# Performance work log

Measured on AMD Instinct MI355X. Metric: run time of the kernel, lower is better.

Reference implementation:

```python
import jax, jax.numpy as jnp
import numpy as np

B, C, D, J = 8, 2048, 128, 128

def setup_inputs() -> dict:
    key = jax.random.key(0)
    ks = jax.random.split(key, 24)
    s = 0.02
    inp = {
        "operation_features": jax.random.normal(ks[0], (B, C, D), jnp.float32),
        "relations": jax.random.randint(ks[1], (B, C - 2, 2), 0, C, jnp.int64),
        "begins_idx": jax.random.randint(ks[2], (B, J), 0, C, jnp.int64),
        "ends_idx": jax.random.randint(ks[3], (B, J), 0, C, jnp.int64),
        "same_type_mask": (jax.random.uniform(ks[4], (B, C, C)) > 0.5).astype(jnp.float32),
        # BeginEndEncoder
        "W_begin": jax.random.normal(ks[5], (D, D), jnp.float32) * s,
        "b_begin": jnp.zeros((D,), jnp.float32),
        "W_end": jax.random.normal(ks[6], (D, D), jnp.float32) * s,
        "b_end": jnp.zeros((D,), jnp.float32),
        # OperationTimeRelationEncoder.mix: Linear(3D -> D)
        "W_mix3": jax.random.normal(ks[7], (3 * D, D), jnp.float32) * s,
        "b_mix3": jnp.zeros((D,), jnp.float32),
        # SelfAttention (hidden_dim = D)
        "W_qkv": jax.random.normal(ks[8], (D, 3 * D), jnp.float32) * s,
        "b_qkv": jnp.zeros((3 * D,), jnp.float32),
        "w_score": jax.random.normal(ks[9], (2 * D,), jnp.float32) * s,
        "b_score": jnp.zeros((), jnp.float32),
        "W_out": jax.random.normal(ks[10], (D, D), jnp.float32) * s,
        "b_out": jnp.zeros((D,), jnp.float32),
        # block mix: Linear(2D -> D)
        "W_mix2": jax.random.normal(ks[11], (2 * D, D), jnp.float32) * s,
        "b_mix2": jnp.zeros((D,), jnp.float32),
    }
    return inp

def _gather_ops(ops, idx):
    # ops: [B,C,D], idx: [B,M] -> [B,M,D]  (torch.gather along dim 1 with expanded index)
    Bb, _, Dd = ops.shape
    M = idx.shape[1]
    return jnp.take_along_axis(ops, jnp.broadcast_to(idx[:, :, None], (Bb, M, Dd)), axis=1)

def reference(operation_features, relations, begins_idx, ends_idx, same_type_mask,
              W_begin, b_begin, W_end, b_end, W_mix3, b_mix3,
              W_qkv, b_qkv, w_score, b_score, W_out, b_out, W_mix2, b_mix2):
    ops = operation_features
    Dd = ops.shape[-1]
    # --- OperationTimeRelationEncoder ---
    pred = _gather_ops(ops, relations[..., 0])      # [B,C-2,D]
    succ = _gather_ops(ops, relations[..., 1])      # [B,C-2,D]
    concated = jnp.concatenate([ops[:, :-2, :], pred, succ], axis=-1)  # [B,C-2,3D]
    mixed = concated @ W_mix3 + b_mix3              # [B,C-2,D]
    begin_f = _gather_ops(ops, begins_idx) @ W_begin + b_begin  # [B,J,D]
    end_f = _gather_ops(ops, ends_idx) @ W_end + b_end
    begin = jnp.mean(begin_f, axis=1)               # [B,D]
    end = jnp.mean(end_f, axis=1)
    seq = jnp.concatenate([mixed, begin[:, None, :], end[:, None, :]], axis=1)  # [B,C,D]
    # --- SelfAttention (GAT-style additive score, decomposed to avoid CxCx2h blowup) ---
    qkv = ops @ W_qkv + b_qkv                       # [B,C,3D]
    q, k, v = jnp.split(qkv, 3, axis=-1)
    sq = q @ w_score[:Dd]                           # [B,C]  q_i . w_q
    sk = k @ w_score[Dd:]                           # [B,C]  k_j . w_k
    scores = jax.nn.leaky_relu(sq[:, :, None] + sk[:, None, :] + b_score)  # [B,C,C]
    attn = jax.nn.softmax(scores * same_type_mask, axis=-1)                # multiplicative mask, as in torch
    weighted = jnp.einsum('bij,bjd->bid', attn, v)  # [B,C,D]
    same_type = weighted @ W_out + b_out            # [B,C,D]
    # --- final mix ---
    return jnp.concatenate([seq, same_type], axis=-1) @ W_mix2 + b_mix2  # [B,C,D]
```

## Files before the change

kernel.cpp:

```cpp
#include <hip/hip_runtime.h>
#include <cstddef>

typedef __bf16 bf16;
typedef __bf16 bf16x4 __attribute__((ext_vector_type(4)));
typedef __bf16 bf16x8 __attribute__((ext_vector_type(8)));
typedef float  f32x4  __attribute__((ext_vector_type(4)));

#define MFMA16(a, b, c) __builtin_amdgcn_mfma_f32_16x16x32_bf16((a), (b), (c), 0, 0, 0)

#define BB 8
#define CC 2048
#define DD 128
#define JJN 128

#define WS_PK    ((size_t)0)
#define WS_OATT  ((size_t)4194304)
#define WS_OPS16 ((size_t)8388608)
#define WS_SQF   ((size_t)12582912)
#define WS_SKF   ((size_t)12648448)
#define WS_G1T   ((size_t)12713984)
#define WS_G2T   ((size_t)12746752)
#define WS_G3T   ((size_t)12779520)
#define WS_WCT   ((size_t)12812288)
#define WS_GBT   ((size_t)12845056)
#define WS_GET   ((size_t)12877824)
#define WS_UQK   ((size_t)12910592)
#define WS_BBM   ((size_t)12911104)
#define WS_BBB   ((size_t)12911616)
#define WS_BBE   ((size_t)12912128)
#define WS_SC    ((size_t)12912640)

__global__ __launch_bounds__(256) void k_prepcast(
    const float* __restrict__ ops, bf16* __restrict__ ops16,
    const float* __restrict__ Wmix3, const float* __restrict__ Wmix2,
    const float* __restrict__ Wout,  const float* __restrict__ Wbegin,
    const float* __restrict__ Wend,  const float* __restrict__ Wqkv,
    const float* __restrict__ bqkv,  const float* __restrict__ wscore,
    const float* __restrict__ bscore,const float* __restrict__ bmix3,
    const float* __restrict__ bout,  const float* __restrict__ bmix2,
    const float* __restrict__ bbegin,const float* __restrict__ bend,
    bf16* __restrict__ G1T, bf16* __restrict__ G2T, bf16* __restrict__ G3T,
    bf16* __restrict__ WCT, bf16* __restrict__ GBT, bf16* __restrict__ GET,
    bf16* __restrict__ uqk, float* __restrict__ BBM, float* __restrict__ BBB,
    float* __restrict__ BBE, float* __restrict__ sc)
{
    __shared__ bf16  LshT[128 * 132];
    __shared__ float Rsh[128 * 8];
    int wg = blockIdx.x;
    int t  = threadIdx.x;

    if (wg < 1024) {
        size_t i = (size_t)wg * 256 + t;
        f32x4 a = *(const f32x4*)(ops + i * 8);
        f32x4 b = *(const f32x4*)(ops + i * 8 + 4);
        bf16x8 o;
        #pragma unroll
        for (int e = 0; e < 4; ++e) { o[e] = (bf16)a[e]; o[4 + e] = (bf16)b[e]; }
        *(bf16x8*)(ops16 + i * 8) = o;
        return;
    }
    if (wg < 1120) {
        int id  = wg - 1024;
        int mat = id >> 4, sub = id & 15;
        const float* L; const float* R; bf16* O;
        switch (mat) {
            case 0: L = Wmix3;           R = Wmix2;           O = G1T; break;
            case 1: L = Wmix3 + 128*128; R = Wmix2;           O = G2T; break;
            case 2: L = Wmix3 + 256*128; R = Wmix2;           O = G3T; break;
            case 3: L = Wout;            R = Wmix2 + 128*128; O = WCT; break;
            case 4: L = Wbegin;          R = Wmix2;           O = GBT; break;
            default:L = Wend;            R = Wmix2;           O = GET; break;
        }
        int e0 = sub * 8;
        #pragma unroll
        for (int pass = 0; pass < 16; ++pass) {
            int idx = pass * 256 + t;
            int d   = idx >> 5;
            int f0  = (idx & 31) * 4;
            f32x4 v = *(const f32x4*)(L + d * 128 + f0);
            #pragma unroll
            for (int jj = 0; jj < 4; ++jj)
                LshT[(f0 + jj) * 132 + d] = (bf16)v[jj];
        }
        #pragma unroll
        for (int pass = 0; pass < 4; ++pass) {
            int idx = pass * 256 + t;
            int f   = idx >> 3;
            int ee  = idx & 7;
            Rsh[f * 8 + ee] = R[f * 128 + e0 + ee];
        }
        __syncthreads();
        int ee = t >> 5;
        int e  = e0 + ee;
        int d0 = (t & 31) * 4;
        float s[4] = {0.f, 0.f, 0.f, 0.f};
        for (int f = 0; f < 128; ++f) {
            bf16x4 lv = *(const bf16x4*)&LshT[f * 132 + d0];
            float rv = Rsh[f * 8 + ee];
            #pragma unroll
            for (int dd = 0; dd < 4; ++dd)
                s[dd] += (float)lv[dd] * rv;
        }
        #pragma unroll
        for (int dd = 0; dd < 4; ++dd)
            O[e * 128 + d0 + dd] = (bf16)s[dd];
        return;
    }
    if (t < 128) {
        int d = t;
        float su = 0.f, sk_ = 0.f;
        for (int e2 = 0; e2 < 128; ++e2) {
            su  += Wqkv[d*384 + e2]       * wscore[e2];
            sk_ += Wqkv[d*384 + 128 + e2] * wscore[128 + e2];
        }
        uqk[d]       = (bf16)su;
        uqk[128 + d] = (bf16)sk_;
        int e = d;
        float bm = 0.f, bon = 0.f, bb_ = 0.f, be_ = 0.f;
        for (int f = 0; f < 128; ++f) {
            float w2a = Wmix2[f*128 + e];
            float w2b = Wmix2[(128+f)*128 + e];
            bm  += bmix3[f]  * w2a;
            bon += bout[f]   * w2b;
            bb_ += bbegin[f] * w2a;
            be_ += bend[f]   * w2a;
        }
        float bm2 = bmix2[e];
        BBM[e] = bm  + bon + bm2;
        BBB[e] = bb_ + bon + bm2;
        BBE[e] = be_ + bon + bm2;
    } else if (t == 128) {
        float cq = 0.f, ck = 0.f;
        for (int e2 = 0; e2 < 128; ++e2) {
            cq += bqkv[e2]       * wscore[e2];
            ck += bqkv[128 + e2] * wscore[128 + e2];
        }
        sc[0] = cq + bscore[0];
        sc[1] = ck;
    }
}

__global__ __launch_bounds__(256) void k_v(
    const bf16* __restrict__ ops16, const float* __restrict__ Wqkv,
    const float* __restrict__ bqkv, const bf16* __restrict__ uqk,
    const float* __restrict__ sc,
    bf16* __restrict__ PK, float* __restrict__ sqf, float* __restrict__ skf)
{
    __shared__ bf16 A[144 * 136];
    int b  = blockIdx.x >> 4;
    int jt = (blockIdx.x & 15) * 128;
    int t  = threadIdx.x;
    #pragma unroll
    for (int pass = 0; pass < 16; ++pass) {
        int idx = pass * 256 + t;
        int d   = idx >> 5;
        int n0  = (idx & 31) * 4;
        f32x4 v = *(const f32x4*)(Wqkv + d*384 + 256 + n0);
        #pragma unroll
        for (int jj = 0; jj < 4; ++jj)
            A[(n0 + jj)*136 + d] = (bf16)v[jj];
    }
    {
        int row = t >> 7, col = t & 127;
        A[(128 + row)*136 + col] = uqk[row*128 + col];
    }
    for (int idx = t; idx < 14*136; idx += 256)
        A[130*136 + idx] = (bf16)0.f;
    __syncthreads();

    int lane = t & 63, w = t >> 6;
    int m = lane & 15, q = lane >> 4;
    f32x4 acc[9][2];
    #pragma unroll
    for (int rb = 0; rb < 9; ++rb)
        #pragma unroll
        for (int cb = 0; cb < 2; ++cb)
            acc[rb][cb] = {0.f, 0.f, 0.f, 0.f};

    const bf16* opsb = ops16 + (size_t)b * CC * DD;
    #pragma unroll
    for (int kc = 0; kc < 4; ++kc) {
        bf16x8 bfr[2];
        #pragma unroll
        for (int cb = 0; cb < 2; ++cb) {
            int j = jt + w*32 + cb*16 + m;
            bfr[cb] = *(const bf16x8*)(opsb + (size_t)j*DD + kc*32 + q*8);
        }
        #pragma unroll
        for (int rb = 0; rb < 9; ++rb) {
            bf16x8 afr = *(const bf16x8*)&A[(rb*16 + m)*136 + kc*32 + q*8];
            acc[rb][0] = MFMA16(afr, bfr[0], acc[rb][0]);
            acc[rb][1] = MFMA16(afr, bfr[1], acc[rb][1]);
        }
    }
    float cqb = sc[0], ckv = sc[1];
    bf16* pkb = PK + (size_t)b * DD * CC;
    #pragma unroll
    for (int cb = 0; cb < 2; ++cb) {
        int j  = jt + w*32 + cb*16 + m;
        int jc = j >> 5, jl = j & 31;
        int qq = jl >> 3, e = jl & 7;
        #pragma unroll
        for (int rb = 0; rb < 8; ++rb) {
            #pragma unroll
            for (int r = 0; r < 4; ++r) {
                float v = acc[rb][cb][r] + bqkv[256 + rb*16 + q*4 + r];
                pkb[((size_t)(((jc*8 + rb)*4 + qq)*16 + (q*4 + r)))*8 + e] = (bf16)v;
            }
        }
        if (q == 0) {
            sqf[b*CC + j] = acc[8][cb][0] + cqb;
            skf[b*CC + j] = acc[8][cb][1] + ckv;
        }
    }
}

struct MaskLd { f32x4 v[4]; };

__device__ __forceinline__ MaskLd stage_load(const float* __restrict__ mrow0,
                                             int st, int lane)
{
    MaskLd L;
    int rr0 = lane >> 4, cc = (lane & 15) * 4;
    const float* src = mrow0 + st * 64 + cc;
    #pragma unroll
    for (int k = 0; k < 4; ++k)
        L.v[k] = __builtin_nontemporal_load(
            (const f32x4*)(src + ((size_t)(rr0 + k * 4)) * CC));
    return L;
}

__device__ __forceinline__ void stage_write(const MaskLd& L, bf16* mb,
                                            int st, int lane)
{
    int rr0 = lane >> 4, cc = (lane & 15) * 4;
    bf16* dst = mb + (st & 1) * 1152;
    #pragma unroll
    for (int k = 0; k < 4; ++k) {
        bf16x4 o;
        #pragma unroll
        for (int e = 0; e < 4; ++e) o[e] = (bf16)L.v[k][e];
        *(bf16x4*)(dst + (rr0 + k * 4) * 72 + cc) = o;
    }
}

__device__ __forceinline__ void load_vb(const bf16* __restrict__ pkb, int jc,
                                        int q, int m, bf16x8 vb[8])
{
    #pragma unroll
    for (int nb = 0; nb < 8; ++nb)
        vb[nb] = *(const bf16x8*)(pkb + ((size_t)(((jc*8 + nb)*4 + q)*16 + m)) * 8);
}

__device__ __forceinline__ void substep(const bf16* mb, const float* skb,
    int st, int sub, int q, int m, float sq, const bf16x8 vb[8],
    float& lsum, f32x4 acc[8])
{
    bf16x8 mk = *(const bf16x8*)(mb + (st & 1) * 1152 + m * 72 + sub * 32 + q * 8);
    int jo = st * 64 + sub * 32 + q * 8;
    f32x4 s0 = *(const f32x4*)(skb + jo);
    f32x4 s1 = *(const f32x4*)(skb + jo + 4);
    float sks[8] = {s0[0], s0[1], s0[2], s0[3], s1[0], s1[1], s1[2], s1[3]};
    bf16x8 a;
    #pragma unroll
    for (int e = 0; e < 8; ++e) {
        float tv = sq + sks[e];
        float lr = fmaxf(tv, 0.01f * tv);
        float z  = lr * (float)mk[e];
        float p  = __expf(z);
        lsum += p;
        a[e] = (bf16)p;
    }
    #pragma unroll
    for (int nb = 0; nb < 8; ++nb)
        acc[nb] = MFMA16(a, vb[nb], acc[nb]);
}

__global__ __launch_bounds__(256, 3) void k_att(
    const float* __restrict__ mask, const bf16* __restrict__ PK,
    const float* __restrict__ sqf, const float* __restrict__ skf,
    bf16* __restrict__ Oatt)
{
    __shared__ __align__(16) char smem[34048];
    int t    = threadIdx.x;
    int lane = t & 63, w = t >> 6;
    int b    = blockIdx.x & 7;
    int i0   = (blockIdx.x >> 3) << 4;
    int m = lane & 15, q = lane >> 4;

    bf16*  mbuf = (bf16*)(smem + w * 4608);
    float* skb  = (float*)(smem + 18432 + w * 2048);

    {
        const float* src = skf + b*CC + w*512;
        f32x4 v0 = *(const f32x4*)(src + lane*4);
        f32x4 v1 = *(const f32x4*)(src + 256 + lane*4);
        *(f32x4*)(skb + lane*4) = v0;
        *(f32x4*)(skb + 256 + lane*4) = v1;
    }
    float sq = sqf[b*CC + i0 + m];
    const float* mrow0 = mask + ((size_t)(b*CC + i0))*CC + w*512;
    const bf16*  pkb   = PK + (size_t)b * DD * CC;
    int jc0 = w * 16;

    f32x4 acc[8];
    #pragma unroll
    for (int nb = 0; nb < 8; ++nb) acc[nb] = {0.f, 0.f, 0.f, 0.f};
    float lsum = 0.f;

    MaskLd L0 = stage_load(mrow0, 0, lane);
    stage_write(L0, mbuf, 0, lane);
    bf16x8 vbA[8], vbB[8];
    load_vb(pkb, jc0, q, m, vbA);

    for (int st = 0; st < 8; ++st) {
        MaskLd Ln;
        if (st < 7) Ln = stage_load(mrow0, st + 1, lane);
        load_vb(pkb, jc0 + st*2 + 1, q, m, vbB);
        substep(mbuf, skb, st, 0, q, m, sq, vbA, lsum, acc);
        if (st < 7) load_vb(pkb, jc0 + st*2 + 2, q, m, vbA);
        substep(mbuf, skb, st, 1, q, m, sq, vbB, lsum, acc);
        if (st < 7) stage_write(Ln, mbuf, st + 1, lane);
    }

    __syncthreads();
    float* Osh = (float*)smem;
    float* Lsh = (float*)(smem + 33792);
    lsum += __shfl_xor(lsum, 16, 64);
    lsum += __shfl_xor(lsum, 32, 64);
    if (q == 0) Lsh[w*16 + m] = lsum;
    #pragma unroll
    for (int nb = 0; nb < 8; ++nb)
        #pragma unroll
        for (int r = 0; r < 4; ++r)
            Osh[(w*16 + q*4 + r)*132 + nb*16 + m] = acc[nb][r];
    __syncthreads();

    int r  = t >> 4;
    int c0 = (t & 15) * 8;
    float l = Lsh[r] + Lsh[16 + r] + Lsh[32 + r] + Lsh[48 + r];
    float inv = 1.0f / l;
    bf16x8 o;
    #pragma unroll
    for (int e = 0; e < 8; ++e) {
        float s = Osh[r*132 + c0 + e] + Osh[(16 + r)*132 + c0 + e]
                + Osh[(32 + r)*132 + c0 + e] + Osh[(48 + r)*132 + c0 + e];
        o[e] = (bf16)(s * inv);
    }
    *(bf16x8*)(Oatt + ((size_t)(b*CC) + i0 + r)*DD + c0) = o;
}

__global__ __launch_bounds__(256) void k_epi(
    const bf16* __restrict__ ops16, const int* __restrict__ relations,
    const bf16* __restrict__ Oatt,
    const bf16* __restrict__ G1T, const bf16* __restrict__ G2T,
    const bf16* __restrict__ G3T, const bf16* __restrict__ WCT,
    const float* __restrict__ BBM, float* __restrict__ out)
{
    __shared__ bf16 Abuf[32 * 136];
    __shared__ bf16 Bbuf[128 * 136];
    int b  = blockIdx.x >> 6;
    int c0 = (blockIdx.x & 63) * 32;
    int t  = threadIdx.x;
    int lane = t & 63, w = t >> 6;
    int m = lane & 15, q = lane >> 4;

    f32x4 acc[2][2];
    #pragma unroll
    for (int rb = 0; rb < 2; ++rb)
        #pragma unroll
        for (int cb = 0; cb < 2; ++cb)
            acc[rb][cb] = {0.f, 0.f, 0.f, 0.f};

    const bf16* Bsrc[4] = {G1T, G2T, G3T, WCT};
    int arow = t >> 3, ao = (t & 7) * 16;
    int brow = t >> 1, bo = (t & 1) * 64;
    int c = c0 + arow;

    for (int term = 0; term < 4; ++term) {
        const bf16* src;
        if (term == 0)      src = ops16 + ((size_t)(b*CC + c)) * DD;
        else if (term == 3) src = Oatt  + ((size_t)(b*CC + c)) * DD;
        else {
            int ridx = relations[((size_t)b*(CC-2) + min(c, CC-3))*2 + (term - 1)];
            src = ops16 + ((size_t)(b*CC) + ridx) * DD;
        }
        *(uint4*)&Abuf[arow*136 + ao]     = *(const uint4*)(src + ao);
        *(uint4*)&Abuf[arow*136 + ao + 8] = *(const uint4*)(src + ao + 8);

        const uint4* bs = (const uint4*)(Bsrc[term] + brow*128 + bo);
        uint4* bd = (uint4*)&Bbuf[brow*136 + bo];
        #pragma unroll
        for (int ii = 0; ii < 8; ++ii) bd[ii] = bs[ii];
        __syncthreads();

        #pragma unroll
        for (int kc = 0; kc < 4; ++kc) {
            bf16x8 bfr[2];
            #pragma unroll
            for (int cb = 0; cb < 2; ++cb)
                bfr[cb] = *(const bf16x8*)&Bbuf[(w*32 + cb*16 + m)*136 + kc*32 + q*8];
            #pragma unroll
            for (int rb = 0; rb < 2; ++rb) {
                bf16x8 afr = *(const bf16x8*)&Abuf[(rb*16 + m)*136 + kc*32 + q*8];
                acc[rb][0] = MFMA16(afr, bfr[0], acc[rb][0]);
                acc[rb][1] = MFMA16(afr, bfr[1], acc[rb][1]);
            }
        }
        __syncthreads();
    }
    #pragma unroll
    for (int cb = 0; cb < 2; ++cb) {
        int col = w*32 + cb*16 + m;
        float bias = BBM[col];
        #pragma unroll
        for (int rb = 0; rb < 2; ++rb) {
            #pragma unroll
            for (int r = 0; r < 4; ++r) {
                int cg = c0 + rb*16 + q*4 + r;
                if (cg < CC - 2)
                    out[((size_t)(b*CC) + cg)*DD + col] = acc[rb][cb][r] + bias;
            }
        }
    }
}

__global__ __launch_bounds__(128) void k_edge(
    const bf16* __restrict__ ops16, const int* __restrict__ begins,
    const int* __restrict__ ends, const bf16* __restrict__ Oatt,
    const bf16* __restrict__ GBT, const bf16* __restrict__ GET,
    const bf16* __restrict__ WCT, const float* __restrict__ BBB,
    const float* __restrict__ BBE, float* __restrict__ out)
{
    __shared__ float meanv[128];
    int b = blockIdx.x >> 1, which = blockIdx.x & 1;
    int t = threadIdx.x;
    const int* idx = which ? (ends + b*JJN) : (begins + b*JJN);
    const bf16* opsb = ops16 + (size_t)b * CC * DD;
    float s = 0.f;
    for (int j = 0; j < JJN; ++j) {
        int r = idx[j];
        s += (float)opsb[(size_t)r*DD + t];
    }
    meanv[t] = s * (1.0f / (float)JJN);
    __syncthreads();
    const bf16* G  = which ? GET : GBT;
    const float* Bv = which ? BBE : BBB;
    const bf16* orow = Oatt + ((size_t)b*CC + (CC - 2 + which)) * DD;
    float a = Bv[t];
    const bf16* gr = G + t*128;
    const bf16* wr = WCT + t*128;
    for (int d = 0; d < 128; ++d) {
        a += meanv[d] * (float)gr[d];
        a += (float)orow[d] * (float)wr[d];
    }
    out[((size_t)b*CC + (CC - 2 + which))*DD + t] = a;
}

extern "C" void kernel_launch(void* const* d_in, const int* in_sizes, int n_in,
                              void* d_out, int out_size, void* d_ws, size_t ws_size,
                              hipStream_t stream)
{
    const float* ops      = (const float*)d_in[0];
    const int*  relations = (const int*)d_in[1];
    const int*  begins    = (const int*)d_in[2];
    const int*  ends      = (const int*)d_in[3];
    const float* mask     = (const float*)d_in[4];
    const float* Wbegin   = (const float*)d_in[5];
    const float* bbegin   = (const float*)d_in[6];
    const float* Wend     = (const float*)d_in[7];
    const float* bend     = (const float*)d_in[8];
    const float* Wmix3    = (const float*)d_in[9];
    const float* bmix3    = (const float*)d_in[10];
    const float* Wqkv     = (const float*)d_in[11];
    const float* bqkv     = (const float*)d_in[12];
    const float* wscore   = (const float*)d_in[13];
    const float* bscore   = (const float*)d_in[14];
    const float* Wout     = (const float*)d_in[15];
    const float* bout     = (const float*)d_in[16];
    const float* Wmix2    = (const float*)d_in[17];
    const float* bmix2    = (const float*)d_in[18];
    float* outp = (float*)d_out;

    char* ws = (char*)d_ws;
    bf16*  PK    = (bf16*)(ws + WS_PK);
    bf16*  Oatt  = (bf16*)(ws + WS_OATT);
    bf16*  OPS16 = (bf16*)(ws + WS_OPS16);
    float* sqf   = (float*)(ws + WS_SQF);
    float* skf   = (float*)(ws + WS_SKF);
    bf16*  G1T   = (bf16*)(ws + WS_G1T);
    bf16*  G2T   = (bf16*)(ws + WS_G2T);
    bf16*  G3T   = (bf16*)(ws + WS_G3T);
    bf16*  WCT   = (bf16*)(ws + WS_WCT);
    bf16*  GBT   = (bf16*)(ws + WS_GBT);
    bf16*  GET   = (bf16*)(ws + WS_GET);
    bf16*  UQK   = (bf16*)(ws + WS_UQK);
    float* BBM   = (float*)(ws + WS_BBM);
    float* BBB   = (float*)(ws + WS_BBB);
    float* BBE   = (float*)(ws + WS_BBE);
    float* SC    = (float*)(ws + WS_SC);

    k_prepcast<<<dim3(1121), dim3(256), 0, stream>>>(
        ops, OPS16,
        Wmix3, Wmix2, Wout, Wbegin, Wend, Wqkv, bqkv, wscore, bscore,
        bmix3, bout, bmix2, bbegin, bend,
        G1T, G2T, G3T, WCT, GBT, GET, UQK, BBM, BBB, BBE, SC);

    k_v<<<dim3(128), dim3(256), 0, stream>>>(
        OPS16, Wqkv, bqkv, UQK, SC, PK, sqf, skf);

    k_att<<<dim3(1024), dim3(256), 0, stream>>>(
        mask, PK, sqf, skf, Oatt);

    k_epi<<<dim3(512), dim3(256), 0, stream>>>(
        OPS16, relations, Oatt, G1T, G2T, G3T, WCT, BBM, outp);

    k_edge<<<dim3(16), dim3(128), 0, stream>>>(
        OPS16, begins, ends, Oatt, GBT, GET, WCT, BBB, BBE, outp);
}
```

Before: 313.0 us.

## Deepen mask prefetch to three stages, stage PK stores through LDS, fuse edge kernel

The attention kernel now keeps two mask stages in flight in registers and uses a triple-buffered LDS ring instead of a double buffer. This hides more HBM latency on the 134MB mask stream, at the cost of more registers, and the occupancy hint of 3 is dropped. The k_v kernel now packs its PK output in shared memory and writes it out with coalesced 16-byte stores instead of scattered 2-byte stores. The begin/end edge kernel is folded into k_epi as 8 extra blocks, which removes one launch.

```diff
diff --git a/kernel.cpp b/kernel.cpp
--- a/kernel.cpp
+++ b/kernel.cpp
@@ -194,24 +194,35 @@
         }
     }
     float cqb = sc[0], ckv = sc[1];
-    bf16* pkb = PK + (size_t)b * DD * CC;
     #pragma unroll
     for (int cb = 0; cb < 2; ++cb) {
-        int j  = jt + w*32 + cb*16 + m;
-        int jc = j >> 5, jl = j & 31;
-        int qq = jl >> 3, e = jl & 7;
+        int j = jt + w*32 + cb*16 + m;
+        if (q == 0) {
+            sqf[b*CC + j] = acc[8][cb][0] + cqb;
+            skf[b*CC + j] = acc[8][cb][1] + ckv;
+        }
+    }
+    __syncthreads();
+    bf16* pack = A;
+    #pragma unroll
+    for (int cb = 0; cb < 2; ++cb) {
+        int qq_base = cb*2 + (m>>3);
+        int e       = m & 7;
         #pragma unroll
         for (int rb = 0; rb < 8; ++rb) {
             #pragma unroll
             for (int r = 0; r < 4; ++r) {
                 float v = acc[rb][cb][r] + bqkv[256 + rb*16 + q*4 + r];
-                pkb[((size_t)(((jc*8 + rb)*4 + qq)*16 + (q*4 + r)))*8 + e] = (bf16)v;
+                pack[w*4096 + rb*512 + qq_base*128 + (q*4+r)*8 + e] = (bf16)v;
             }
         }
-        if (q == 0) {
-            sqf[b*CC + j] = acc[8][cb][0] + cqb;
-            skf[b*CC + j] = acc[8][cb][1] + ckv;
-        }
+    }
+    __syncthreads();
+    bf16* pkb = PK + (size_t)b * DD * CC + (size_t)jt * 128;
+    #pragma unroll
+    for (int pass = 0; pass < 8; ++pass) {
+        int lidx = pass * 256 + t;
+        *(uint4*)(pkb + (size_t)lidx * 8) = *(const uint4*)&pack[lidx * 8];
     }
 }
 
@@ -231,10 +242,10 @@
 }
 
 __device__ __forceinline__ void stage_write(const MaskLd& L, bf16* mb,
-                                            int st, int lane)
+                                            int buf, int lane)
 {
     int rr0 = lane >> 4, cc = (lane & 15) * 4;
-    bf16* dst = mb + (st & 1) * 1152;
+    bf16* dst = mb + buf * 1152;
     #pragma unroll
     for (int k = 0; k < 4; ++k) {
         bf16x4 o;
@@ -253,10 +264,10 @@
 }
 
 __device__ __forceinline__ void substep(const bf16* mb, const float* skb,
-    int st, int sub, int q, int m, float sq, const bf16x8 vb[8],
+    int buf, int st, int sub, int q, int m, float sq, const bf16x8 vb[8],
     float& lsum, f32x4 acc[8])
 {
-    bf16x8 mk = *(const bf16x8*)(mb + (st & 1) * 1152 + m * 72 + sub * 32 + q * 8);
+    bf16x8 mk = *(const bf16x8*)(mb + buf * 1152 + m * 72 + sub * 32 + q * 8);
     int jo = st * 64 + sub * 32 + q * 8;
     f32x4 s0 = *(const f32x4*)(skb + jo);
     f32x4 s1 = *(const f32x4*)(skb + jo + 4);
@@ -276,20 +287,20 @@
         acc[nb] = MFMA16(a, vb[nb], acc[nb]);
 }
 
-__global__ __launch_bounds__(256, 3) void k_att(
+__global__ __launch_bounds__(256) void k_att(
     const float* __restrict__ mask, const bf16* __restrict__ PK,
     const float* __restrict__ sqf, const float* __restrict__ skf,
     bf16* __restrict__ Oatt)
 {
-    __shared__ __align__(16) char smem[34048];
+    __shared__ __align__(16) char smem[35840];
     int t    = threadIdx.x;
     int lane = t & 63, w = t >> 6;
     int b    = blockIdx.x & 7;
     int i0   = (blockIdx.x >> 3) << 4;
     int m = lane & 15, q = lane >> 4;
 
-    bf16*  mbuf = (bf16*)(smem + w * 4608);
-    float* skb  = (float*)(smem + 18432 + w * 2048);
+    bf16*  mbuf = (bf16*)(smem + w * 6912);
+    float* skb  = (float*)(smem + 27648 + w * 2048);
 
     {
         const float* src = skf + b*CC + w*512;
@@ -308,19 +319,25 @@
     for (int nb = 0; nb < 8; ++nb) acc[nb] = {0.f, 0.f, 0.f, 0.f};
     float lsum = 0.f;
 
-    MaskLd L0 = stage_load(mrow0, 0, lane);
-    stage_write(L0, mbuf, 0, lane);
+    {   MaskLd r0 = stage_load(mrow0, 0, lane);
+        stage_write(r0, mbuf, 0, lane); }
+    MaskLd r1 = stage_load(mrow0, 1, lane);
+    MaskLd r2 = stage_load(mrow0, 2, lane);
+    MaskLd r3;
     bf16x8 vbA[8], vbB[8];
     load_vb(pkb, jc0, q, m, vbA);
 
+    int bm = 0;
     for (int st = 0; st < 8; ++st) {
-        MaskLd Ln;
-        if (st < 7) Ln = stage_load(mrow0, st + 1, lane);
+        if (st + 3 < 8) r3 = stage_load(mrow0, st + 3, lane);
         load_vb(pkb, jc0 + st*2 + 1, q, m, vbB);
-        substep(mbuf, skb, st, 0, q, m, sq, vbA, lsum, acc);
+        substep(mbuf, skb, bm, st, 0, q, m, sq, vbA, lsum, acc);
         if (st < 7) load_vb(pkb, jc0 + st*2 + 2, q, m, vbA);
-        substep(mbuf, skb, st, 1, q, m, sq, vbB, lsum, acc);
-        if (st < 7) stage_write(Ln, mbuf, st + 1, lane);
+        substep(mbuf, skb, bm, st, 1, q, m, sq, vbB, lsum, acc);
+        int bw = bm + 1; if (bw == 3) bw = 0;
+        if (st + 1 < 8) stage_write(r1, mbuf, bw, lane);
+        r1 = r2; r2 = r3;
+        bm = bw;
     }
 
     __syncthreads();
@@ -352,16 +369,49 @@
 
 __global__ __launch_bounds__(256) void k_epi(
     const bf16* __restrict__ ops16, const int* __restrict__ relations,
+    const int* __restrict__ begins, const int* __restrict__ ends,
     const bf16* __restrict__ Oatt,
     const bf16* __restrict__ G1T, const bf16* __restrict__ G2T,
     const bf16* __restrict__ G3T, const bf16* __restrict__ WCT,
-    const float* __restrict__ BBM, float* __restrict__ out)
+    const bf16* __restrict__ GBT, const bf16* __restrict__ GET,
+    const float* __restrict__ BBM, const float* __restrict__ BBB,
+    const float* __restrict__ BBE, float* __restrict__ out)
 {
     __shared__ bf16 Abuf[32 * 136];
     __shared__ bf16 Bbuf[128 * 136];
+    int t  = threadIdx.x;
+
+    if (blockIdx.x >= 512) {
+        __shared__ float meanv[2][128];
+        int eidx  = (blockIdx.x - 512) * 2 + (t >> 7);
+        int b     = eidx >> 1, which = eidx & 1;
+        int tl    = t & 127;
+        const int* idx = which ? (ends + b*JJN) : (begins + b*JJN);
+        const bf16* opsb = ops16 + (size_t)b * CC * DD;
+        float s = 0.f;
+        for (int j = 0; j < JJN; ++j) {
+            int rr = idx[j];
+            s += (float)opsb[(size_t)rr*DD + tl];
+        }
+        meanv[t >> 7][tl] = s * (1.0f / (float)JJN);
+        __syncthreads();
+        const bf16* G   = which ? GET : GBT;
+        const float* Bv = which ? BBE : BBB;
+        const bf16* orow = Oatt + ((size_t)b*CC + (CC - 2 + which)) * DD;
+        float a = Bv[tl];
+        const bf16* gr = G + tl*128;
+        const bf16* wr = WCT + tl*128;
+        const float* mv = meanv[t >> 7];
+        for (int d = 0; d < 128; ++d) {
+            a += mv[d] * (float)gr[d];
+            a += (float)orow[d] * (float)wr[d];
+        }
+        out[((size_t)b*CC + (CC - 2 + which))*DD + tl] = a;
+        return;
+    }
+
     int b  = blockIdx.x >> 6;
     int c0 = (blockIdx.x & 63) * 32;
-    int t  = threadIdx.x;
     int lane = t & 63, w = t >> 6;
     int m = lane & 15, q = lane >> 4;
 
@@ -423,38 +473,6 @@
             }
         }
     }
-}
-
-__global__ __launch_bounds__(128) void k_edge(
-    const bf16* __restrict__ ops16, const int* __restrict__ begins,
-    const int* __restrict__ ends, const bf16* __restrict__ Oatt,
-    const bf16* __restrict__ GBT, const bf16* __restrict__ GET,
-    const bf16* __restrict__ WCT, const float* __restrict__ BBB,
-    const float* __restrict__ BBE, float* __restrict__ out)
-{
-    __shared__ float meanv[128];
-    int b = blockIdx.x >> 1, which = blockIdx.x & 1;
-    int t = threadIdx.x;
-    const int* idx = which ? (ends + b*JJN) : (begins + b*JJN);
-    const bf16* opsb = ops16 + (size_t)b * CC * DD;
-    float s = 0.f;
-    for (int j = 0; j < JJN; ++j) {
-        int r = idx[j];
-        s += (float)opsb[(size_t)r*DD + t];
-    }
-    meanv[t] = s * (1.0f / (float)JJN);
-    __syncthreads();
-    const bf16* G  = which ? GET : GBT;
-    const float* Bv = which ? BBE : BBB;
-    const bf16* orow = Oatt + ((size_t)b*CC + (CC - 2 + which)) * DD;
-    float a = Bv[t];
-    const bf16* gr = G + t*128;
-    const bf16* wr = WCT + t*128;
-    for (int d = 0; d < 128; ++d) {
-        a += meanv[d] * (float)gr[d];
-        a += (float)orow[d] * (float)wr[d];
-    }
-    out[((size_t)b*CC + (CC - 2 + which))*DD + t] = a;
 }
 
 extern "C" void kernel_launch(void* const* d_in, const int* in_sizes, int n_in,
@@ -512,9 +530,7 @@
     k_att<<<dim3(1024), dim3(256), 0, stream>>>(
         mask, PK, sqf, skf, Oatt);
 
-    k_epi<<<dim3(512), dim3(256), 0, stream>>>(
-        OPS16, relations, Oatt, G1T, G2T, G3T, WCT, BBM, outp);
-
-    k_edge<<<dim3(16), dim3(128), 0, stream>>>(
-        OPS16, begins, ends, Oatt, GBT, GET, WCT, BBB, BBE, outp);
-}
+    k_epi<<<dim3(520), dim3(256), 0, stream>>>(
+        OPS16, relations, begins, ends, Oatt,
+        G1T, G2T, G3T, WCT, GBT, GET, BBM, BBB, BBE, outp);
+}
```

Measured after the change: 296.2 us. -5.4%, faster.
